# Optimization experiments

Hardware: AMD Instinct MI355X
Metric: run time of the kernel (lower is better)

The kernel has to match this reference:

```python
import jax, jax.numpy as jnp
import numpy as np

N, E, DIM, HID, LAYERS = 100000, 600000, 128, 256, 2
LN_EPS = 1e-5


def setup_inputs() -> dict:
    key = jax.random.key(0)
    ks = jax.random.split(key, 16)
    h = jax.random.normal(ks[0], (N, DIM), dtype=jnp.float32)
    edge_index = jax.random.randint(ks[1], (E, 2), 0, N, dtype=jnp.int64)
    edge_attr = jax.random.uniform(ks[2], (E, 1), dtype=jnp.float32)
    s = 0.02
    # edge MLP: Linear(2*DIM+1, HID) -> GELU -> Linear(HID, 1) -> Sigmoid
    edge_w1 = jax.random.normal(ks[3], (LAYERS, 2 * DIM + 1, HID), dtype=jnp.float32) * s
    edge_b1 = jnp.zeros((LAYERS, HID), dtype=jnp.float32)
    edge_w2 = jax.random.normal(ks[4], (LAYERS, HID, 1), dtype=jnp.float32) * s
    edge_b2 = jnp.zeros((LAYERS, 1), dtype=jnp.float32)
    # node MLP: Linear(2*DIM, HID) -> GELU -> Linear(HID, DIM)
    node_w1 = jax.random.normal(ks[5], (LAYERS, 2 * DIM, HID), dtype=jnp.float32) * s
    node_b1 = jnp.zeros((LAYERS, HID), dtype=jnp.float32)
    node_w2 = jax.random.normal(ks[6], (LAYERS, HID, DIM), dtype=jnp.float32) * s
    node_b2 = jnp.zeros((LAYERS, DIM), dtype=jnp.float32)
    ln_g = jnp.ones((LAYERS, DIM), dtype=jnp.float32)
    ln_b = jnp.zeros((LAYERS, DIM), dtype=jnp.float32)
    return {"h": h, "edge_index": edge_index, "edge_attr": edge_attr,
            "edge_w1": edge_w1, "edge_b1": edge_b1, "edge_w2": edge_w2, "edge_b2": edge_b2,
            "node_w1": node_w1, "node_b1": node_b1, "node_w2": node_w2, "node_b2": node_b2,
            "ln_g": ln_g, "ln_b": ln_b}


def _layernorm(x, g, b):
    mu = jnp.mean(x, axis=-1, keepdims=True)
    var = jnp.mean(jnp.square(x - mu), axis=-1, keepdims=True)
    return (x - mu) * jax.lax.rsqrt(var + LN_EPS) * g + b


def reference(h, edge_index, edge_attr, edge_w1, edge_b1, edge_w2, edge_b2,
              node_w1, node_b1, node_w2, node_b2, ln_g, ln_b):
    src = edge_index[:, 0]
    dst = edge_index[:, 1]
    n = h.shape[0]
    for i in range(LAYERS):
        h_src = h[src]                                  # [E, DIM]
        h_dst = h[dst]                                  # [E, DIM]
        x = jnp.concatenate([h_src, h_dst, edge_attr], axis=-1)  # [E, 2*DIM+1]
        g1 = jax.nn.gelu(x @ edge_w1[i] + edge_b1[i], approximate=False)
        gate = jax.nn.sigmoid(g1 @ edge_w2[i] + edge_b2[i])       # [E, 1]
        msg = h_src * gate                              # [E, DIM]
        agg = jax.ops.segment_sum(msg, dst, num_segments=n)       # [N, DIM]
        den = jax.ops.segment_sum(gate, dst, num_segments=n)      # [N, 1]
        agg = agg / jnp.maximum(den, 1e-6)
        u = jnp.concatenate([h, agg], axis=-1)          # [N, 2*DIM]
        upd = jax.nn.gelu(u @ node_w1[i] + node_b1[i], approximate=False) @ node_w2[i] + node_b2[i]
        h = _layernorm(h + upd, ln_g[i], ln_b[i])
    return h
```

## Files before the change

### kernel.cpp

```cpp
#include <hip/hip_runtime.h>
#include <math.h>

#define NNODE 100000
#define NEDGE 600000
#define DIM 128
#define HID 256
#define NLAYERS 2

typedef short bf16x8 __attribute__((ext_vector_type(8)));
typedef short bf16x4 __attribute__((ext_vector_type(4)));
typedef float f32x4 __attribute__((ext_vector_type(4)));

#define WK 136
#define WLD 264
#define LUTN 2048

__device__ __forceinline__ short f2bf(float x) {
    union { float f; unsigned u; } v; v.f = x;
    unsigned r = v.u + 0x7FFFu + ((v.u >> 16) & 1u);
    return (short)(r >> 16);
}
__device__ __forceinline__ float bf2f(short s) {
    union { unsigned u; float f; } v; v.u = ((unsigned)(unsigned short)s) << 16;
    return v.f;
}
__device__ __forceinline__ float u_lo_f(unsigned u) {
    union { unsigned u; float f; } v; v.u = u << 16; return v.f;
}
__device__ __forceinline__ float u_hi_f(unsigned u) {
    union { unsigned u; float f; } v; v.u = u & 0xFFFF0000u; return v.f;
}
__device__ __forceinline__ float gelu_erf(float x) {
    float z = x * 0.70710678118654752f;
    float az = fabsf(z);
    float t = __builtin_amdgcn_rcpf(1.0f + 0.3275911f * az);
    float y = t * (0.254829592f + t * (-0.284496736f + t * (1.421413741f +
              t * (-1.453152027f + t * 1.061405429f))));
    float e = __expf(-az * az);
    float er = 1.0f - y * e;
    er = copysignf(er, z);
    return 0.5f * x * (1.0f + er);
}
__device__ __forceinline__ float lut_look(const float* __restrict__ lut, float x) {
    float t = fmaf(x, 128.f, 1024.5f);
    t = fminf(fmaxf(t, 0.f), 2047.f);
    return lut[(int)t];
}

__global__ void prep_weights(const float* __restrict__ ew1,
                             const float* __restrict__ eb1,
                             const float* __restrict__ ew2,
                             const float* __restrict__ nw1,
                             const float* __restrict__ nw2,
                             const float* __restrict__ h0,
                             const int* __restrict__ ei,
                             short* __restrict__ pW,
                             short* __restrict__ nW1T,
                             short* __restrict__ nW2T,
                             float* __restrict__ w1a_p,
                             float* __restrict__ b1_p,
                             float* __restrict__ w2_p,
                             short* __restrict__ hb,
                             float* __restrict__ luts,
                             int* __restrict__ deg)
{
    int idx = blockIdx.x * 256 + threadIdx.x;
    const int SZ1 = NLAYERS * 512 * 128;
    const int SZ2 = NLAYERS * 256 * 256;
    const int SZ3 = NLAYERS * 128 * 256;
    const int SZ4 = NLAYERS * 256;
    const int SZH = NNODE * DIM / 8;
    if (idx < SZ1) {
        int L = idx / (512 * 128); int rr = idx - L * 512 * 128;
        int r = rr >> 7, k = rr & 127;
        int srow = (r < 256) ? k : 128 + k;
        int scol = (r < 256) ? r : r - 256;
        pW[(size_t)L * 512 * WK + r * WK + k] = f2bf(ew1[(size_t)L * 257 * 256 + srow * 256 + scol]);
        return;
    }
    idx -= SZ1;
    if (idx < SZ2) {
        int L = idx >> 16, r = idx & 65535, n = r >> 8, k = r & 255;
        nW1T[(size_t)L * 256 * WLD + n * WLD + k] = f2bf(nw1[(size_t)L * 256 * 256 + k * 256 + n]);
        return;
    }
    idx -= SZ2;
    if (idx < SZ3) {
        int L = idx >> 15, r = idx & 32767, n = r >> 8, k = r & 255;
        nW2T[(size_t)L * 128 * WLD + n * WLD + k] = f2bf(nw2[(size_t)L * 256 * 128 + k * 128 + n]);
        return;
    }
    idx -= SZ3;
    if (idx < SZ4) {
        int L = idx >> 8, c = idx & 255;
        int cs = (c & ~63) | ((c & 3) * 16 + ((c >> 2) & 15));
        w1a_p[idx] = ew1[(size_t)L * 257 * 256 + 256 * 256 + cs];
        b1_p[idx]  = eb1[(size_t)L * 256 + cs];
        w2_p[idx]  = ew2[(size_t)L * 256 + cs];
        return;
    }
    idx -= SZ4;
    if (idx < SZH) {
        const float4* p = (const float4*)(h0 + (size_t)idx * 8);
        float4 a = p[0], b = p[1];
        bf16x8 t;
        t[0] = f2bf(a.x); t[1] = f2bf(a.y); t[2] = f2bf(a.z); t[3] = f2bf(a.w);
        t[4] = f2bf(b.x); t[5] = f2bf(b.y); t[6] = f2bf(b.z); t[7] = f2bf(b.w);
        *(bf16x8*)(hb + (size_t)idx * 8) = t;
        return;
    }
    idx -= SZH;
    if (idx < 2 * LUTN) {
        int i = idx & (LUTN - 1);
        float x = (float)(i - 1024) * (1.0f / 128.0f);
        float v;
        if (idx < LUTN) {
            v = 0.5f * x * (1.0f + erff(x * 0.70710678118654752f));
        } else {
            v = 1.0f / (1.0f + expf(-x));
        }
        luts[idx] = v;
        return;
    }
    idx -= 2 * LUTN;
    if (idx < NEDGE) {
        atomicAdd(&deg[ei[2 * idx + 1]], 1);
    }
}

__global__ __launch_bounds__(1024)
void csr_scan(const int* __restrict__ deg, int* __restrict__ rowptr, int* __restrict__ cursor) {
    __shared__ int wsum[16];
    __shared__ int carry_s;
    const int tid = threadIdx.x, lane = tid & 63, wv = tid >> 6;
    if (tid == 0) carry_s = 0;
    __syncthreads();
    for (int base = 0; base < NNODE; base += 4096) {
        int i0 = base + tid * 4;
        int v0 = 0, v1 = 0, v2 = 0, v3 = 0;
        if (i0 + 3 < NNODE) {
            int4 q = *(const int4*)(deg + i0);
            v0 = q.x; v1 = q.y; v2 = q.z; v3 = q.w;
        } else if (i0 < NNODE) {
            v0 = deg[i0];
            if (i0 + 1 < NNODE) v1 = deg[i0 + 1];
            if (i0 + 2 < NNODE) v2 = deg[i0 + 2];
        }
        int tsum = v0 + v1 + v2 + v3;
        int x = tsum;
#pragma unroll
        for (int off = 1; off < 64; off <<= 1) {
            int y = __shfl_up(x, off);
            if (lane >= off) x += y;
        }
        if (lane == 63) wsum[wv] = x;
        __syncthreads();
        if (wv == 0) {
            int s = (lane < 16) ? wsum[lane] : 0;
#pragma unroll
            for (int off = 1; off < 16; off <<= 1) {
                int y = __shfl_up(s, off);
                if (lane >= off) s += y;
            }
            if (lane < 16) wsum[lane] = s;
        }
        __syncthreads();
        int carry = carry_s;
        int woff = wv ? wsum[wv - 1] : 0;
        int e0 = carry + woff + (x - tsum);
        if (i0 < NNODE)     { rowptr[i0] = e0;                cursor[i0] = e0; }
        if (i0 + 1 < NNODE) { int v = e0 + v0;                rowptr[i0+1] = v; cursor[i0+1] = v; }
        if (i0 + 2 < NNODE) { int v = e0 + v0 + v1;           rowptr[i0+2] = v; cursor[i0+2] = v; }
        if (i0 + 3 < NNODE) { int v = e0 + v0 + v1 + v2;      rowptr[i0+3] = v; cursor[i0+3] = v; }
        int total = wsum[15];
        __syncthreads();
        if (tid == 0) carry_s = carry + total;
        __syncthreads();
    }
    if (tid == 0) rowptr[NNODE] = carry_s;
}

__global__ void csr_scatter(const int* __restrict__ ei, const float* __restrict__ attr,
                            int* __restrict__ cursor, int2* __restrict__ epk) {
    int e = blockIdx.x * 256 + threadIdx.x;
    if (e >= NEDGE) return;
    int s = ei[2 * e], d = ei[2 * e + 1];
    int pos = atomicAdd(&cursor[d], 1);
    int2 pk; pk.x = s; pk.y = __float_as_int(attr[e]);
    epk[pos] = pk;
    if (e == 0) { int2 z; z.x = 0; z.y = 0; epk[NEDGE] = z; }
}

__global__ __launch_bounds__(512, 2)
void proj_kernel(const short* __restrict__ hb,
                 const short* __restrict__ pW,
                 short* __restrict__ Ps,
                 short* __restrict__ Pd)
{
    __shared__ short A[64][WK];
    const int tid = threadIdx.x;
    const int n0 = blockIdx.x * 64;

    for (int idx = tid; idx < 64 * 16; idx += 512) {
        int nl = idx >> 4, q = idx & 15;
        int gn = min(n0 + nl, NNODE - 1);
        *(bf16x8*)&A[nl][q * 8] = *(const bf16x8*)(hb + (size_t)gn * DIM + q * 8);
    }
    __syncthreads();

    const int lane = tid & 63;
    const int wv = tid >> 6;
    const int lrow = lane & 15;
    const int lkg = lane >> 4;

    f32x4 acc[4][4];
#pragma unroll
    for (int mi = 0; mi < 4; ++mi)
#pragma unroll
        for (int ni = 0; ni < 4; ++ni) acc[mi][ni] = (f32x4){0.f, 0.f, 0.f, 0.f};

    const short* xbase = &A[lrow][lkg * 8];
    const short* wbase = pW + (size_t)(wv * 64 + lrow) * WK + lkg * 8;

#pragma unroll
    for (int kt = 0; kt < 4; ++kt) {
        bf16x8 a[4], b[4];
#pragma unroll
        for (int mi = 0; mi < 4; ++mi)
            a[mi] = *(const bf16x8*)(xbase + mi * 16 * WK + kt * 32);
#pragma unroll
        for (int ni = 0; ni < 4; ++ni)
            b[ni] = *(const bf16x8*)(wbase + ni * 16 * WK + kt * 32);
#pragma unroll
        for (int mi = 0; mi < 4; ++mi)
#pragma unroll
            for (int ni = 0; ni < 4; ++ni)
                acc[mi][ni] = __builtin_amdgcn_mfma_f32_16x16x32_bf16(a[mi], b[ni], acc[mi][ni], 0, 0, 0);
    }

    short* dstP = (wv < 4) ? Ps : Pd;
    const int cb = (wv & 3) * 64;
#pragma unroll
    for (int mi = 0; mi < 4; ++mi)
#pragma unroll
        for (int reg = 0; reg < 4; ++reg) {
            int node = n0 + mi * 16 + lkg * 4 + reg;
            bf16x4 t;
            t[0] = f2bf(acc[mi][0][reg]);
            t[1] = f2bf(acc[mi][1][reg]);
            t[2] = f2bf(acc[mi][2][reg]);
            t[3] = f2bf(acc[mi][3][reg]);
            if (node < NNODE)
                *(bf16x4*)(dstP + (size_t)node * 256 + cb + lrow * 4) = t;
        }
}

__global__ __launch_bounds__(256)
void edge_agg(const short* __restrict__ Ps, const short* __restrict__ Pd,
              const short* __restrict__ hb,
              const int2* __restrict__ epk, const int* __restrict__ rowptr,
              const float* __restrict__ w1a_p, const float* __restrict__ b1_p,
              const float* __restrict__ w2_p, const float* __restrict__ b2,
              const float* __restrict__ luts,
              short* __restrict__ u2)
{
    __shared__ float sg[LUTN];
    __shared__ float ss[LUTN];

    const int tid = threadIdx.x;
#pragma unroll
    for (int i = 0; i < LUTN / 256; ++i) {
        sg[tid + i * 256] = luts[tid + i * 256];
        ss[tid + i * 256] = luts[LUTN + tid + i * 256];
    }
    __syncthreads();

    const int node = (blockIdx.x * 256 + tid) >> 6;
    const int lane = tid & 63;

    const int beg = __builtin_amdgcn_readfirstlane(rowptr[node]);
    const int end = __builtin_amdgcn_readfirstlane(rowptr[node + 1]);
    const int d = end - beg;

    const float4 w1av = ((const float4*)w1a_p)[lane];
    const float4 b1v  = ((const float4*)b1_p)[lane];
    const float4 w2v  = ((const float4*)w2_p)[lane];
    const float b2s = b2[0];

    bf16x4 pd = *(const bf16x4*)(Pd + (size_t)node * 256 + lane * 4);
    const float pb0 = bf2f(pd[0]) + b1v.x;
    const float pb1 = bf2f(pd[1]) + b1v.y;
    const float pb2 = bf2f(pd[2]) + b1v.z;
    const float pb3 = bf2f(pd[3]) + b1v.w;

    const int2* ep = epk + beg;
    const int pso = lane * 4;
    const int hvo = lane * 2;

    float ax = 0.f, ay = 0.f, den = 0.f;

    bf16x4 ps_n = (bf16x4){0, 0, 0, 0};
    unsigned hv_n = 0;
    float a_n = 0.f;
    if (d > 0) {
        int2 sa = ep[0];
        int s0 = __builtin_amdgcn_readfirstlane(sa.x);
        a_n = __int_as_float(__builtin_amdgcn_readfirstlane(sa.y));
        ps_n = *(const bf16x4*)(Ps + ((size_t)s0 << 8) + pso);
        hv_n = *(const unsigned*)(hb + ((size_t)s0 << 7) + hvo);
    }
    for (int t = 0; t < d; ++t) {
        bf16x4 ps = ps_n; unsigned hv = hv_n; float a = a_n;
        {
            int2 sa = ep[t + 1];
            int s2 = __builtin_amdgcn_readfirstlane(sa.x);
            a_n = __int_as_float(__builtin_amdgcn_readfirstlane(sa.y));
            ps_n = *(const bf16x4*)(Ps + ((size_t)s2 << 8) + pso);
            hv_n = *(const unsigned*)(hb + ((size_t)s2 << 7) + hvo);
        }
        float x0 = bf2f(ps[0]) + pb0 + a * w1av.x;
        float x1 = bf2f(ps[1]) + pb1 + a * w1av.y;
        float x2 = bf2f(ps[2]) + pb2 + a * w1av.z;
        float x3 = bf2f(ps[3]) + pb3 + a * w1av.w;
        float p = lut_look(sg, x0) * w2v.x + lut_look(sg, x1) * w2v.y +
                  lut_look(sg, x2) * w2v.z + lut_look(sg, x3) * w2v.w;
        p += __shfl_xor(p, 1);
        p += __shfl_xor(p, 2);
        p += __shfl_xor(p, 4);
        p += __shfl_xor(p, 8);
        p += __shfl_xor(p, 16);
        p += __shfl_xor(p, 32);
        float g = lut_look(ss, p + b2s);
        ax = fmaf(g, u_lo_f(hv), ax);
        ay = fmaf(g, u_hi_f(hv), ay);
        den += g;
    }

    float dd = fmaxf(den, 1e-6f);
    float dinv = __builtin_amdgcn_rcpf(dd);
    dinv = dinv * (2.0f - dd * dinv);
    unsigned pk = (((unsigned)(unsigned short)f2bf(ay * dinv)) << 16) |
                  (unsigned)(unsigned short)f2bf(ax * dinv);
    *(unsigned*)(u2 + (size_t)node * 256 + lane * 2) = pk;
}

__global__ __launch_bounds__(256, 4)
void node_mlp(const float* __restrict__ hin,
              const short* __restrict__ hb,
              const short* __restrict__ u2,
              const short* __restrict__ W1T,
              const float* __restrict__ b1,
              const short* __restrict__ W2T,
              const float* __restrict__ b2,
              const float* __restrict__ lng, const float* __restrict__ lnb,
              float* __restrict__ hout, short* __restrict__ hb_out)
{
    __shared__ short U[32][WLD];
    __shared__ short G[32][WLD];

    const int tid = threadIdx.x;
    const int n0 = blockIdx.x * 32;
    const int lane = tid & 63;
    const int wv = tid >> 6;

    for (int idx = tid; idx < 32 * 32; idx += 256) {
        int nl = idx >> 5, q = idx & 31;
        const short* src = (q < 16) ? (hb + (size_t)(n0 + nl) * DIM + q * 8)
                                    : (u2 + (size_t)(n0 + nl) * 256 + (q - 16) * 8);
        *(bf16x8*)&U[nl][q * 8] = *(const bf16x8*)src;
    }
    __syncthreads();

    const int lrow = lane & 15;
    const int lkg = lane >> 4;

    {
        const int n0w = wv * 64;
        f32x4 acc1[2][4];
#pragma unroll
        for (int mi = 0; mi < 2; ++mi)
#pragma unroll
            for (int ni = 0; ni < 4; ++ni) acc1[mi][ni] = (f32x4){0.f, 0.f, 0.f, 0.f};

        const short* xbase = &U[lrow][lkg * 8];
        const short* wbase = W1T + (size_t)(n0w + lrow) * WLD + lkg * 8;
#pragma unroll
        for (int kt = 0; kt < 8; ++kt) {
            bf16x8 a[2], b[4];
#pragma unroll
            for (int mi = 0; mi < 2; ++mi)
                a[mi] = *(const bf16x8*)(xbase + mi * 16 * WLD + kt * 32);
#pragma unroll
            for (int ni = 0; ni < 4; ++ni)
                b[ni] = *(const bf16x8*)(wbase + ni * 16 * WLD + kt * 32);
#pragma unroll
            for (int mi = 0; mi < 2; ++mi)
#pragma unroll
                for (int ni = 0; ni < 4; ++ni)
                    acc1[mi][ni] = __builtin_amdgcn_mfma_f32_16x16x32_bf16(a[mi], b[ni], acc1[mi][ni], 0, 0, 0);
        }

        float b1v[4];
#pragma unroll
        for (int ni = 0; ni < 4; ++ni) b1v[ni] = b1[n0w + ni * 16 + lrow];
#pragma unroll
        for (int mi = 0; mi < 2; ++mi)
#pragma unroll
            for (int ni = 0; ni < 4; ++ni)
#pragma unroll
                for (int reg = 0; reg < 4; ++reg) {
                    int row = mi * 16 + lkg * 4 + reg;
                    int col = n0w + ni * 16 + lrow;
                    G[row][col] = f2bf(gelu_erf(acc1[mi][ni][reg] + b1v[ni]));
                }
    }
    __syncthreads();

    float* R = (float*)&U[0][0];
    {
        f32x4 acc2[2][2];
#pragma unroll
        for (int mi = 0; mi < 2; ++mi)
#pragma unroll
            for (int ni = 0; ni < 2; ++ni) acc2[mi][ni] = (f32x4){0.f, 0.f, 0.f, 0.f};

        const short* xbase = &G[lrow][lkg * 8];
        const short* wbase = W2T + (size_t)(wv * 32 + lrow) * WLD + lkg * 8;
#pragma unroll
        for (int kt = 0; kt < 8; ++kt) {
            bf16x8 a[2], b[2];
#pragma unroll
            for (int mi = 0; mi < 2; ++mi)
                a[mi] = *(const bf16x8*)(xbase + mi * 16 * WLD + kt * 32);
#pragma unroll
            for (int ni = 0; ni < 2; ++ni)
                b[ni] = *(const bf16x8*)(wbase + ni * 16 * WLD + kt * 32);
#pragma unroll
            for (int mi = 0; mi < 2; ++mi)
#pragma unroll
                for (int ni = 0; ni < 2; ++ni)
                    acc2[mi][ni] = __builtin_amdgcn_mfma_f32_16x16x32_bf16(a[mi], b[ni], acc2[mi][ni], 0, 0, 0);
        }

        float b2v[2];
#pragma unroll
        for (int ni = 0; ni < 2; ++ni) b2v[ni] = b2[wv * 32 + ni * 16 + lrow];
#pragma unroll
        for (int mi = 0; mi < 2; ++mi)
#pragma unroll
            for (int ni = 0; ni < 2; ++ni)
#pragma unroll
                for (int reg = 0; reg < 4; ++reg) {
                    int row = mi * 16 + lkg * 4 + reg;
                    int col = wv * 32 + ni * 16 + lrow;
                    R[row * 132 + col] = acc2[mi][ni][reg] + b2v[ni];
                }
    }
    __syncthreads();

#pragma unroll
    for (int ii = 0; ii < 8; ++ii) {
        int nl = wv * 8 + ii;
        int gn = n0 + nl;
        float rx = R[nl * 132 + lane * 2 + 0];
        float ry = R[nl * 132 + lane * 2 + 1];
        const float2 hh = *(const float2*)(hin + (size_t)gn * DIM + lane * 2);
        float vx = rx + hh.x, vy = ry + hh.y;
        float s = vx + vy;
#pragma unroll
        for (int off = 32; off > 0; off >>= 1) s += __shfl_xor(s, off);
        float mu = s * (1.0f / 128.0f);
        float dx = vx - mu, dy = vy - mu;
        float q = dx * dx + dy * dy;
#pragma unroll
        for (int off = 32; off > 0; off >>= 1) q += __shfl_xor(q, off);
        float inv = rsqrtf(q * (1.0f / 128.0f) + 1e-5f);
        const float2 gg = *(const float2*)(lng + lane * 2);
        const float2 bb = *(const float2*)(lnb + lane * 2);
        float ox = dx * inv * gg.x + bb.x;
        float oy = dy * inv * gg.y + bb.y;
        *(float2*)(hout + (size_t)gn * DIM + lane * 2) = make_float2(ox, oy);
        unsigned pk = ((unsigned)(unsigned short)f2bf(oy) << 16) |
                      (unsigned)(unsigned short)f2bf(ox);
        *(unsigned*)(hb_out + (size_t)gn * DIM + lane * 2) = pk;
    }
}

extern "C" void kernel_launch(void* const* d_in, const int* in_sizes, int n_in,
                              void* d_out, int out_size, void* d_ws, size_t ws_size,
                              hipStream_t stream) {
    const float* h0   = (const float*)d_in[0];
    const int*   ei   = (const int*)d_in[1];
    const float* attr = (const float*)d_in[2];
    const float* ew1  = (const float*)d_in[3];
    const float* eb1  = (const float*)d_in[4];
    const float* ew2  = (const float*)d_in[5];
    const float* eb2  = (const float*)d_in[6];
    const float* nw1  = (const float*)d_in[7];
    const float* nb1  = (const float*)d_in[8];
    const float* nw2  = (const float*)d_in[9];
    const float* nb2  = (const float*)d_in[10];
    const float* lng  = (const float*)d_in[11];
    const float* lnb  = (const float*)d_in[12];

    float* hout = (float*)d_out;

    char* p = (char*)d_ws;
    int*   rowptr = (int*)p;               p += sizeof(int) * (NNODE + 4);
    int*   cursor = (int*)p;               p += sizeof(int) * (NNODE + 4);
    int*   deg    = (int*)p;               p += sizeof(int) * (NNODE + 4);
    int2*  epk    = (int2*)p;              p += sizeof(int2) * (NEDGE + 1);
    short* hb     = (short*)p;             p += sizeof(short) * (size_t)NNODE * DIM;
    short* Ps     = (short*)p;             p += sizeof(short) * (size_t)NNODE * 256;
    short* Pd     = (short*)p;             p += sizeof(short) * (size_t)NNODE * 256;
    short* u2     = Pd;
    short* pW     = (short*)p;             p += sizeof(short) * (size_t)NLAYERS * 512 * WK;
    short* nW1T   = (short*)p;             p += sizeof(short) * (size_t)NLAYERS * 256 * WLD;
    short* nW2T   = (short*)p;             p += sizeof(short) * (size_t)NLAYERS * 128 * WLD;
    float* w1a_p  = (float*)p;             p += sizeof(float) * NLAYERS * 256;
    float* b1_p   = (float*)p;             p += sizeof(float) * NLAYERS * 256;
    float* w2_p   = (float*)p;             p += sizeof(float) * NLAYERS * 256;
    float* luts   = (float*)p;             p += sizeof(float) * 2 * LUTN;

    const int PREP_TOTAL = NLAYERS * 512 * 128 + NLAYERS * 256 * 256 +
                           NLAYERS * 128 * 256 + NLAYERS * 256 + NNODE * DIM / 8 +
                           2 * LUTN + NEDGE;

    hipMemsetAsync(deg, 0, (NNODE + 1) * sizeof(int), stream);
    prep_weights<<<(PREP_TOTAL + 255) / 256, 256, 0, stream>>>(
        ew1, eb1, ew2, nw1, nw2, h0, ei, pW, nW1T, nW2T, w1a_p, b1_p, w2_p, hb, luts, deg);
    csr_scan<<<1, 1024, 0, stream>>>(deg, rowptr, cursor);
    csr_scatter<<<(NEDGE + 255) / 256, 256, 0, stream>>>(ei, attr, cursor, epk);

    for (int L = 0; L < NLAYERS; ++L) {
        const float* hin = (L == 0) ? h0 : hout;
        proj_kernel<<<(NNODE + 63) / 64, 512, 0, stream>>>(
            hb, pW + (size_t)L * 512 * WK, Ps, Pd);
        edge_agg<<<NNODE / 4, 256, 0, stream>>>(
            Ps, Pd, hb, epk, rowptr,
            w1a_p + (size_t)L * 256, b1_p + (size_t)L * 256,
            w2_p + (size_t)L * 256, eb2 + L, luts, u2);
        node_mlp<<<NNODE / 32, 256, 0, stream>>>(
            hin, hb, u2,
            nW1T + (size_t)L * 256 * WLD, nb1 + (size_t)L * 256,
            nW2T + (size_t)L * 128 * WLD, nb2 + (size_t)L * 128,
            lng + (size_t)L * DIM, lnb + (size_t)L * DIM,
            hout, hb);
    }
}
```

Measured before the change: 535.9 us.

## Store source projection in FP8 and enlarge node MLP tiles to 64 rows

The per-source projection Ps is written as packed FP8 instead of bf16, halving the bytes gathered per edge in edge_agg, and is decoded with hardware fp8-to-f32 conversions. The node MLP now processes 64 nodes per block with a single reused shared buffer instead of separate U and G arrays, adding a synchronisation before GELU outputs overwrite the inputs and bounds clamping for the tail block. FP8 storage reduces the precision of the gate pre-activation, which may affect accuracy.

```diff
diff --git a/kernel.cpp b/kernel.cpp
--- a/kernel.cpp
+++ b/kernel.cpp
@@ -10,6 +10,7 @@
 typedef short bf16x8 __attribute__((ext_vector_type(8)));
 typedef short bf16x4 __attribute__((ext_vector_type(4)));
 typedef float f32x4 __attribute__((ext_vector_type(4)));
+typedef float f32x2 __attribute__((ext_vector_type(2)));
 
 #define WK 136
 #define WLD 264
@@ -194,7 +195,7 @@
 __global__ __launch_bounds__(512, 2)
 void proj_kernel(const short* __restrict__ hb,
                  const short* __restrict__ pW,
-                 short* __restrict__ Ps,
+                 unsigned char* __restrict__ Ps8,
                  short* __restrict__ Pd)
 {
     __shared__ short A[64][WK];
@@ -238,25 +239,37 @@
                 acc[mi][ni] = __builtin_amdgcn_mfma_f32_16x16x32_bf16(a[mi], b[ni], acc[mi][ni], 0, 0, 0);
     }
 
-    short* dstP = (wv < 4) ? Ps : Pd;
     const int cb = (wv & 3) * 64;
-#pragma unroll
-    for (int mi = 0; mi < 4; ++mi)
-#pragma unroll
-        for (int reg = 0; reg < 4; ++reg) {
-            int node = n0 + mi * 16 + lkg * 4 + reg;
-            bf16x4 t;
-            t[0] = f2bf(acc[mi][0][reg]);
-            t[1] = f2bf(acc[mi][1][reg]);
-            t[2] = f2bf(acc[mi][2][reg]);
-            t[3] = f2bf(acc[mi][3][reg]);
-            if (node < NNODE)
-                *(bf16x4*)(dstP + (size_t)node * 256 + cb + lrow * 4) = t;
-        }
+    if (wv < 4) {
+#pragma unroll
+        for (int mi = 0; mi < 4; ++mi)
+#pragma unroll
+            for (int reg = 0; reg < 4; ++reg) {
+                int node = n0 + mi * 16 + lkg * 4 + reg;
+                int w = __builtin_amdgcn_cvt_pk_fp8_f32(acc[mi][0][reg], acc[mi][1][reg], 0, false);
+                w = __builtin_amdgcn_cvt_pk_fp8_f32(acc[mi][2][reg], acc[mi][3][reg], w, true);
+                if (node < NNODE)
+                    *(unsigned*)(Ps8 + (size_t)node * 256 + cb + lrow * 4) = (unsigned)w;
+            }
+    } else {
+#pragma unroll
+        for (int mi = 0; mi < 4; ++mi)
+#pragma unroll
+            for (int reg = 0; reg < 4; ++reg) {
+                int node = n0 + mi * 16 + lkg * 4 + reg;
+                bf16x4 t;
+                t[0] = f2bf(acc[mi][0][reg]);
+                t[1] = f2bf(acc[mi][1][reg]);
+                t[2] = f2bf(acc[mi][2][reg]);
+                t[3] = f2bf(acc[mi][3][reg]);
+                if (node < NNODE)
+                    *(bf16x4*)(Pd + (size_t)node * 256 + cb + lrow * 4) = t;
+            }
+    }
 }
 
 __global__ __launch_bounds__(256)
-void edge_agg(const short* __restrict__ Ps, const short* __restrict__ Pd,
+void edge_agg(const unsigned char* __restrict__ Ps8, const short* __restrict__ Pd,
               const short* __restrict__ hb,
               const int2* __restrict__ epk, const int* __restrict__ rowptr,
               const float* __restrict__ w1a_p, const float* __restrict__ b1_p,
@@ -299,29 +312,31 @@
 
     float ax = 0.f, ay = 0.f, den = 0.f;
 
-    bf16x4 ps_n = (bf16x4){0, 0, 0, 0};
+    unsigned ps_n = 0;
     unsigned hv_n = 0;
     float a_n = 0.f;
     if (d > 0) {
         int2 sa = ep[0];
         int s0 = __builtin_amdgcn_readfirstlane(sa.x);
         a_n = __int_as_float(__builtin_amdgcn_readfirstlane(sa.y));
-        ps_n = *(const bf16x4*)(Ps + ((size_t)s0 << 8) + pso);
+        ps_n = *(const unsigned*)(Ps8 + ((size_t)s0 << 8) + pso);
         hv_n = *(const unsigned*)(hb + ((size_t)s0 << 7) + hvo);
     }
     for (int t = 0; t < d; ++t) {
-        bf16x4 ps = ps_n; unsigned hv = hv_n; float a = a_n;
+        unsigned psu = ps_n; unsigned hv = hv_n; float a = a_n;
         {
             int2 sa = ep[t + 1];
             int s2 = __builtin_amdgcn_readfirstlane(sa.x);
             a_n = __int_as_float(__builtin_amdgcn_readfirstlane(sa.y));
-            ps_n = *(const bf16x4*)(Ps + ((size_t)s2 << 8) + pso);
+            ps_n = *(const unsigned*)(Ps8 + ((size_t)s2 << 8) + pso);
             hv_n = *(const unsigned*)(hb + ((size_t)s2 << 7) + hvo);
         }
-        float x0 = bf2f(ps[0]) + pb0 + a * w1av.x;
-        float x1 = bf2f(ps[1]) + pb1 + a * w1av.y;
-        float x2 = bf2f(ps[2]) + pb2 + a * w1av.z;
-        float x3 = bf2f(ps[3]) + pb3 + a * w1av.w;
+        f32x2 plo = __builtin_amdgcn_cvt_pk_f32_fp8((int)psu, false);
+        f32x2 phi = __builtin_amdgcn_cvt_pk_f32_fp8((int)psu, true);
+        float x0 = plo[0] + pb0 + a * w1av.x;
+        float x1 = plo[1] + pb1 + a * w1av.y;
+        float x2 = phi[0] + pb2 + a * w1av.z;
+        float x3 = phi[1] + pb3 + a * w1av.w;
         float p = lut_look(sg, x0) * w2v.x + lut_look(sg, x1) * w2v.y +
                   lut_look(sg, x2) * w2v.z + lut_look(sg, x3) * w2v.w;
         p += __shfl_xor(p, 1);
@@ -355,98 +370,102 @@
               const float* __restrict__ lng, const float* __restrict__ lnb,
               float* __restrict__ hout, short* __restrict__ hb_out)
 {
-    __shared__ short U[32][WLD];
-    __shared__ short G[32][WLD];
+    __shared__ short U[64][WLD];
 
     const int tid = threadIdx.x;
-    const int n0 = blockIdx.x * 32;
+    const int n0 = blockIdx.x * 64;
     const int lane = tid & 63;
     const int wv = tid >> 6;
 
-    for (int idx = tid; idx < 32 * 32; idx += 256) {
+    for (int idx = tid; idx < 64 * 32; idx += 256) {
         int nl = idx >> 5, q = idx & 31;
-        const short* src = (q < 16) ? (hb + (size_t)(n0 + nl) * DIM + q * 8)
-                                    : (u2 + (size_t)(n0 + nl) * 256 + (q - 16) * 8);
+        int gn = min(n0 + nl, NNODE - 1);
+        const short* src = (q < 16) ? (hb + (size_t)gn * DIM + q * 8)
+                                    : (u2 + (size_t)gn * 256 + (q - 16) * 8);
         *(bf16x8*)&U[nl][q * 8] = *(const bf16x8*)src;
     }
     __syncthreads();
 
     const int lrow = lane & 15;
     const int lkg = lane >> 4;
-
+    const int n0w = wv * 64;
+
+    f32x4 acc1[4][4];
+#pragma unroll
+    for (int mi = 0; mi < 4; ++mi)
+#pragma unroll
+        for (int ni = 0; ni < 4; ++ni) acc1[mi][ni] = (f32x4){0.f, 0.f, 0.f, 0.f};
     {
-        const int n0w = wv * 64;
-        f32x4 acc1[2][4];
-#pragma unroll
-        for (int mi = 0; mi < 2; ++mi)
-#pragma unroll
-            for (int ni = 0; ni < 4; ++ni) acc1[mi][ni] = (f32x4){0.f, 0.f, 0.f, 0.f};
-
         const short* xbase = &U[lrow][lkg * 8];
         const short* wbase = W1T + (size_t)(n0w + lrow) * WLD + lkg * 8;
 #pragma unroll
         for (int kt = 0; kt < 8; ++kt) {
-            bf16x8 a[2], b[4];
-#pragma unroll
-            for (int mi = 0; mi < 2; ++mi)
+            bf16x8 a[4], b[4];
+#pragma unroll
+            for (int mi = 0; mi < 4; ++mi)
                 a[mi] = *(const bf16x8*)(xbase + mi * 16 * WLD + kt * 32);
 #pragma unroll
             for (int ni = 0; ni < 4; ++ni)
                 b[ni] = *(const bf16x8*)(wbase + ni * 16 * WLD + kt * 32);
 #pragma unroll
-            for (int mi = 0; mi < 2; ++mi)
+            for (int mi = 0; mi < 4; ++mi)
 #pragma unroll
                 for (int ni = 0; ni < 4; ++ni)
                     acc1[mi][ni] = __builtin_amdgcn_mfma_f32_16x16x32_bf16(a[mi], b[ni], acc1[mi][ni], 0, 0, 0);
         }
-
+    }
+    __syncthreads();
+
+    {
         float b1v[4];
 #pragma unroll
         for (int ni = 0; ni < 4; ++ni) b1v[ni] = b1[n0w + ni * 16 + lrow];
 #pragma unroll
-        for (int mi = 0; mi < 2; ++mi)
+        for (int mi = 0; mi < 4; ++mi)
 #pragma unroll
             for (int ni = 0; ni < 4; ++ni)
 #pragma unroll
                 for (int reg = 0; reg < 4; ++reg) {
                     int row = mi * 16 + lkg * 4 + reg;
                     int col = n0w + ni * 16 + lrow;
-                    G[row][col] = f2bf(gelu_erf(acc1[mi][ni][reg] + b1v[ni]));
+                    U[row][col] = f2bf(gelu_erf(acc1[mi][ni][reg] + b1v[ni]));
                 }
+    }
+    __syncthreads();
+
+    f32x4 acc2[4][2];
+#pragma unroll
+    for (int mi = 0; mi < 4; ++mi)
+#pragma unroll
+        for (int ni = 0; ni < 2; ++ni) acc2[mi][ni] = (f32x4){0.f, 0.f, 0.f, 0.f};
+    {
+        const short* xbase = &U[lrow][lkg * 8];
+        const short* wbase = W2T + (size_t)(wv * 32 + lrow) * WLD + lkg * 8;
+#pragma unroll
+        for (int kt = 0; kt < 8; ++kt) {
+            bf16x8 a[4], b[2];
+#pragma unroll
+            for (int mi = 0; mi < 4; ++mi)
+                a[mi] = *(const bf16x8*)(xbase + mi * 16 * WLD + kt * 32);
+#pragma unroll
+            for (int ni = 0; ni < 2; ++ni)
+                b[ni] = *(const bf16x8*)(wbase + ni * 16 * WLD + kt * 32);
+#pragma unroll
+            for (int mi = 0; mi < 4; ++mi)
+#pragma unroll
+                for (int ni = 0; ni < 2; ++ni)
+                    acc2[mi][ni] = __builtin_amdgcn_mfma_f32_16x16x32_bf16(a[mi], b[ni], acc2[mi][ni], 0, 0, 0);
+        }
     }
     __syncthreads();
 
     float* R = (float*)&U[0][0];
     {
-        f32x4 acc2[2][2];
-#pragma unroll
-        for (int mi = 0; mi < 2; ++mi)
-#pragma unroll
-            for (int ni = 0; ni < 2; ++ni) acc2[mi][ni] = (f32x4){0.f, 0.f, 0.f, 0.f};
-
-        const short* xbase = &G[lrow][lkg * 8];
-        const short* wbase = W2T + (size_t)(wv * 32 + lrow) * WLD + lkg * 8;
-#pragma unroll
-        for (int kt = 0; kt < 8; ++kt) {
-            bf16x8 a[2], b[2];
-#pragma unroll
-            for (int mi = 0; mi < 2; ++mi)
-                a[mi] = *(const bf16x8*)(xbase + mi * 16 * WLD + kt * 32);
-#pragma unroll
-            for (int ni = 0; ni < 2; ++ni)
-                b[ni] = *(const bf16x8*)(wbase + ni * 16 * WLD + kt * 32);
-#pragma unroll
-            for (int mi = 0; mi < 2; ++mi)
-#pragma unroll
-                for (int ni = 0; ni < 2; ++ni)
-                    acc2[mi][ni] = __builtin_amdgcn_mfma_f32_16x16x32_bf16(a[mi], b[ni], acc2[mi][ni], 0, 0, 0);
-        }
-
         float b2v[2];
 #pragma unroll
         for (int ni = 0; ni < 2; ++ni) b2v[ni] = b2[wv * 32 + ni * 16 + lrow];
 #pragma unroll
-        for (int mi = 0; mi < 2; ++mi)
+        for (int mi = 0; mi < 4; ++mi)
 #pragma unroll
             for (int ni = 0; ni < 2; ++ni)
 #pragma unroll
@@ -459,12 +478,13 @@
     __syncthreads();
 
 #pragma unroll
-    for (int ii = 0; ii < 8; ++ii) {
-        int nl = wv * 8 + ii;
+    for (int ii = 0; ii < 16; ++ii) {
+        int nl = wv * 16 + ii;
         int gn = n0 + nl;
+        int gnc = min(gn, NNODE - 1);
         float rx = R[nl * 132 + lane * 2 + 0];
         float ry = R[nl * 132 + lane * 2 + 1];
-        const float2 hh = *(const float2*)(hin + (size_t)gn * DIM + lane * 2);
+        const float2 hh = *(const float2*)(hin + (size_t)gnc * DIM + lane * 2);
         float vx = rx + hh.x, vy = ry + hh.y;
         float s = vx + vy;
 #pragma unroll
@@ -475,14 +495,16 @@
 #pragma unroll
         for (int off = 32; off > 0; off >>= 1) q += __shfl_xor(q, off);
         float inv = rsqrtf(q * (1.0f / 128.0f) + 1e-5f);
-        const float2 gg = *(const float2*)(lng + lane * 2);
-        const float2 bb = *(const float2*)(lnb + lane * 2);
-        float ox = dx * inv * gg.x + bb.x;
-        float oy = dy * inv * gg.y + bb.y;
-        *(float2*)(hout + (size_t)gn * DIM + lane * 2) = make_float2(ox, oy);
-        unsigned pk = ((unsigned)(unsigned short)f2bf(oy) << 16) |
-                      (unsigned)(unsigned short)f2bf(ox);
-        *(unsigned*)(hb_out + (size_t)gn * DIM + lane * 2) = pk;
+        if (gn < NNODE) {
+            const float2 gg = *(const float2*)(lng + lane * 2);
+            const float2 bb = *(const float2*)(lnb + lane * 2);
+            float ox = dx * inv * gg.x + bb.x;
+            float oy = dy * inv * gg.y + bb.y;
+            *(float2*)(hout + (size_t)gn * DIM + lane * 2) = make_float2(ox, oy);
+            unsigned pk = ((unsigned)(unsigned short)f2bf(oy) << 16) |
+                          (unsigned)(unsigned short)f2bf(ox);
+            *(unsigned*)(hb_out + (size_t)gn * DIM + lane * 2) = pk;
+        }
     }
 }
 
@@ -511,7 +533,7 @@
     int*   deg    = (int*)p;               p += sizeof(int) * (NNODE + 4);
     int2*  epk    = (int2*)p;              p += sizeof(int2) * (NEDGE + 1);
     short* hb     = (short*)p;             p += sizeof(short) * (size_t)NNODE * DIM;
-    short* Ps     = (short*)p;             p += sizeof(short) * (size_t)NNODE * 256;
+    unsigned char* Ps8 = (unsigned char*)p; p += (size_t)NNODE * 256;
     short* Pd     = (short*)p;             p += sizeof(short) * (size_t)NNODE * 256;
     short* u2     = Pd;
     short* pW     = (short*)p;             p += sizeof(short) * (size_t)NLAYERS * 512 * WK;
@@ -535,12 +557,12 @@
     for (int L = 0; L < NLAYERS; ++L) {
         const float* hin = (L == 0) ? h0 : hout;
         proj_kernel<<<(NNODE + 63) / 64, 512, 0, stream>>>(
-            hb, pW + (size_t)L * 512 * WK, Ps, Pd);
+            hb, pW + (size_t)L * 512 * WK, Ps8, Pd);
         edge_agg<<<NNODE / 4, 256, 0, stream>>>(
-            Ps, Pd, hb, epk, rowptr,
+            Ps8, Pd, hb, epk, rowptr,
             w1a_p + (size_t)L * 256, b1_p + (size_t)L * 256,
             w2_p + (size_t)L * 256, eb2 + L, luts, u2);
-        node_mlp<<<NNODE / 32, 256, 0, stream>>>(
+        node_mlp<<<(NNODE + 63) / 64, 256, 0, stream>>>(
             hin, hb, u2,
             nW1T + (size_t)L * 256 * WLD, nb1 + (size_t)L * 256,
             nW2T + (size_t)L * 128 * WLD, nb2 + (size_t)L * 128,
```

After: 497.5 us. 1.08x faster.
